# Kernel optimization log

Hardware: AMD Instinct MI355X
Metric: run time of the kernel (lower is better)

## Reference

```python
import jax, jax.numpy as jnp
import numpy as np

BN_EPS = 1e-5

def _conv1x1(x, w, b):
    # x: (B,C,H,W), w: (O,C), b: (O,)
    return jnp.einsum('bchw,oc->bohw', x, w) + b[None, :, None, None]

def setup_inputs() -> dict:
    key = jax.random.key(0)
    ks = jax.random.split(key, 9)
    B, C, H, W = 16, 512, 64, 64
    Ci = C // 2
    x = jax.random.normal(ks[0], (B, C, H, W), dtype=jnp.float32)
    s_in = (2.0 / C) ** 0.5   # kaiming fan_out-ish scale for 1x1 conv
    s_ci = (2.0 / Ci) ** 0.5
    return {
        'x': x,
        'g_w': jax.random.normal(ks[1], (Ci, C), dtype=jnp.float32) * s_in,
        'g_b': jnp.zeros((Ci,), dtype=jnp.float32),
        'theta_w': jax.random.normal(ks[2], (Ci, C), dtype=jnp.float32) * s_in,
        'theta_b': jnp.zeros((Ci,), dtype=jnp.float32),
        'phi_w': jax.random.normal(ks[3], (Ci, C), dtype=jnp.float32) * s_in,
        'phi_b': jnp.zeros((Ci,), dtype=jnp.float32),
        'W_w': jax.random.normal(ks[4], (C, Ci), dtype=jnp.float32) * s_ci,
        'W_b': jnp.zeros((C,), dtype=jnp.float32),
        'bn_gamma': jnp.ones((C,), dtype=jnp.float32),
        'bn_beta': jnp.zeros((C,), dtype=jnp.float32),
    }

def reference(x, g_w, g_b, theta_w, theta_b, phi_w, phi_b, W_w, W_b, bn_gamma, bn_beta):
    B, C, H, W = x.shape
    N = H * W
    g_x = _conv1x1(x, g_w, g_b).reshape(B, -1, N)          # (B, Ci, N)
    theta_x = _conv1x1(x, theta_w, theta_b).reshape(B, -1, N)  # (B, Ci, N)
    phi_x = _conv1x1(x, phi_w, phi_b).reshape(B, -1, N)        # (B, Ci, N)
    # Faithful to source: theta NOT permuted -> f is (B, Ci, Ci) channel attention
    f = jnp.einsum('bcn,bdn->bcd', theta_x, phi_x)
    f_div_C = jax.nn.softmax(f, axis=-1)
    y = jnp.einsum('bcd,bdn->bcn', f_div_C, g_x).reshape(B, -1, H, W)  # (B, Ci, H, W)
    z = _conv1x1(y, W_w, W_b)                              # (B, C, H, W)
    # BatchNorm2d, training mode (batch statistics, biased var as in torch)
    mean = jnp.mean(z, axis=(0, 2, 3), keepdims=True)
    var = jnp.var(z, axis=(0, 2, 3), keepdims=True)
    z = (z - mean) * jax.lax.rsqrt(var + BN_EPS)
    z = z * bn_gamma[None, :, None, None] + bn_beta[None, :, None, None]
    return z + x
```

## Files before the change

### kernel.cpp

```cpp
#include <hip/hip_runtime.h>

typedef __bf16 bf16x8 __attribute__((ext_vector_type(8)));
typedef float f32x4 __attribute__((ext_vector_type(4)));

#define LDK 40
#define NB 16
#define C_ 512
#define CI 256
#define HW 4096
#define KSPLIT 4
#define KCHUNK (HW / KSPLIT)

__device__ __forceinline__ float bf2f(unsigned short u){
  union { unsigned int u; float f; } c; c.u = ((unsigned int)u) << 16; return c.f;
}
__device__ __forceinline__ unsigned short f2bf(float f){
  union { float f; unsigned int u; } c; c.f = f;
  unsigned int u = c.u + 0x7fffu + ((c.u >> 16) & 1u);
  return (unsigned short)(u >> 16);
}
__device__ __forceinline__ float read_val(const void* p, int i, bool f32){
  return f32 ? ((const float*)p)[i] : bf2f(((const unsigned short*)p)[i]);
}


__device__ __forceinline__ void stage_rm(const unsigned short* __restrict__ src, int stride,
                                         unsigned short* dst, int t){
  #pragma unroll
  for (int it = 0; it < 2; ++it){
    int idx = t + it*256;
    int row = idx >> 2;
    int ko  = (idx & 3) * 8;
    *(uint4*)(dst + row*LDK + ko) = *(const uint4*)(src + (size_t)row*stride + ko);
  }
}

__device__ __forceinline__ void stage_tr(const unsigned short* __restrict__ src, int stride,
                                         unsigned short* dst, int t){
  #pragma unroll
  for (int it = 0; it < 2; ++it){
    int idx = t + it*256;
    int row = idx >> 4;
    int co  = (idx & 15) * 8;
    uint4 vv = *(const uint4*)(src + (size_t)row*stride + co);
    unsigned short e[8]; *(uint4*)e = vv;
    #pragma unroll
    for (int k = 0; k < 8; ++k) dst[(co + k)*LDK + row] = e[k];
  }
}

__device__ __forceinline__ void mfma_step(const unsigned short* As, const unsigned short* Bs,
                                          f32x4 acc[4][4], int wm, int wn, int lane){
  const int r = lane & 15, q = lane >> 4;
  bf16x8 a[4], b[4];
  #pragma unroll
  for (int i = 0; i < 4; ++i)
    a[i] = *(const bf16x8*)(As + (wm*64 + 16*i + r)*LDK + 8*q);
  #pragma unroll
  for (int j = 0; j < 4; ++j)
    b[j] = *(const bf16x8*)(Bs + (wn*64 + 16*j + r)*LDK + 8*q);
  #pragma unroll
  for (int i = 0; i < 4; ++i)
    #pragma unroll
    for (int j = 0; j < 4; ++j)
      acc[i][j] = __builtin_amdgcn_mfma_f32_16x16x32_bf16(a[i], b[j], acc[i][j], 0, 0, 0);
}

__global__ __launch_bounds__(256) void k_detect(const unsigned short* __restrict__ x, int* flag){
  const int t = threadIdx.x;
  int cnt = 0;
  for (int i = t; i < 65536; i += 256){
    unsigned short u = x[i];
    if (((u >> 7) & 0xFF) == 0xFF) cnt++;
  }
  __shared__ int red[256];
  red[t] = cnt; __syncthreads();
  for (int s2 = 128; s2 > 0; s2 >>= 1){
    if (t < s2) red[t] += red[t + s2];
    __syncthreads();
  }
  if (t == 0) flag[0] = (red[0] > 0) ? 1 : 0;
}

__global__ __launch_bounds__(256) void k_wconv(const void* tw, const void* pw, const void* gw,
    const void* Ww, const void* gb, const void* tb, const void* pb, const void* Wb,
    const void* gam, const void* bet, const int* __restrict__ flag,
    unsigned short* twh, unsigned short* twl, unsigned short* phh, unsigned short* phl,
    unsigned short* gwc, unsigned short* Wwc, float* biasf){
  const bool f32 = (*flag != 0);
  const int bid = blockIdx.x, t = threadIdx.x;
  if (bid < 2048){
    const int seg = bid >> 9;
    const int i = (bid & 511)*256 + t;
    if (seg == 0){
      float w = read_val(tw, i, f32);
      unsigned short h = f2bf(w);
      twh[i] = h; twl[i] = f2bf(w - bf2f(h));
    } else if (seg == 1){
      float w = read_val(pw, i, f32);
      unsigned short h = f2bf(w);
      phh[i] = h; phl[i] = f2bf(w - bf2f(h));
    } else if (seg == 2){
      gwc[i] = f2bf(read_val(gw, i, f32));
    } else {
      Wwc[i] = f2bf(read_val(Ww, i, f32));
    }
  } else {
    const int i = (bid - 2048)*256 + t;
    if (i < 2304){
      float v;
      if      (i <  256) v = read_val(gb,  i,        f32);
      else if (i <  512) v = read_val(tb,  i - 256,  f32);
      else if (i <  768) v = read_val(pb,  i - 512,  f32);
      else if (i < 1280) v = read_val(Wb,  i - 768,  f32);
      else if (i < 1792) v = read_val(gam, i - 1280, f32);
      else               v = read_val(bet, i - 1792, f32);
      biasf[i] = v;
    }
  }
}

__global__ __launch_bounds__(256) void k_xconv(const void* __restrict__ xraw,
    const int* __restrict__ flag, unsigned short* __restrict__ xh,
    unsigned short* __restrict__ xl, float* __restrict__ s){
  const bool f32 = (*flag != 0);
  const int bc = blockIdx.x, t = threadIdx.x;
  float sum = 0.f;
  if (f32){
    const float* xr = (const float*)xraw + (size_t)bc*HW;
    unsigned short* oh = xh + (size_t)bc*HW;
    unsigned short* ol = xl + (size_t)bc*HW;
    #pragma unroll
    for (int it = 0; it < 4; ++it){
      const int off = it*1024 + t*4;
      f32x4 v = *(const f32x4*)(xr + off);
      unsigned int wh[2], wl[2];
      #pragma unroll
      for (int k = 0; k < 2; ++k){
        unsigned short h0 = f2bf(v[2*k]),   h1 = f2bf(v[2*k+1]);
        unsigned short l0 = f2bf(v[2*k]   - bf2f(h0));
        unsigned short l1 = f2bf(v[2*k+1] - bf2f(h1));
        wh[k] = (unsigned int)h0 | ((unsigned int)h1 << 16);
        wl[k] = (unsigned int)l0 | ((unsigned int)l1 << 16);
      }
      sum += v[0] + v[1] + v[2] + v[3];
      *(uint2*)(oh + off) = make_uint2(wh[0], wh[1]);
      *(uint2*)(ol + off) = make_uint2(wl[0], wl[1]);
    }
  } else {
    const unsigned short* xr = (const unsigned short*)xraw + (size_t)bc*HW;
    #pragma unroll
    for (int it = 0; it < 2; ++it){
      const int off = it*2048 + t*8;
      uint4 raw = *(const uint4*)(xr + off);
      unsigned int wd[4] = {raw.x, raw.y, raw.z, raw.w};
      #pragma unroll
      for (int k = 0; k < 4; ++k)
        sum += bf2f((unsigned short)(wd[k] & 0xffff)) + bf2f((unsigned short)(wd[k] >> 16));
    }
  }
  #pragma unroll
  for (int off = 1; off < 64; off <<= 1) sum += __shfl_xor(sum, off);
  __shared__ float r1[4];
  if ((t & 63) == 0) r1[t >> 6] = sum;
  __syncthreads();
  if (t == 0) s[bc] = r1[0] + r1[1] + r1[2] + r1[3];
}

__global__ __launch_bounds__(256) void k_gram(const void* __restrict__ xraw,
    const unsigned short* __restrict__ xh, const unsigned short* __restrict__ xl,
    const int* __restrict__ flag, float* __restrict__ Gp){
  const bool f32 = (*flag != 0);
  const int b = blockIdx.z, ks = blockIdx.y, tile = blockIdx.x;
  int bm, bn;
  if      (tile < 4){ bm = 0; bn = tile; }
  else if (tile < 7){ bm = 1; bn = tile - 3; }
  else if (tile < 9){ bm = 2; bn = tile - 5; }
  else              { bm = 3; bn = 3; }
  const int t = threadIdx.x, lane = t & 63, w = t >> 6, wm = w >> 1, wn = w & 1;
  __shared__ unsigned short Ah[128*LDK];
  __shared__ unsigned short Al[128*LDK];
  __shared__ unsigned short Bh[128*LDK];
  __shared__ unsigned short Bl[128*LDK];
  f32x4 acc[4][4] = {};
  const bool diag = (bm == bn);
  const unsigned short* xhb = f32 ? (xh + (size_t)b*C_*HW)
                                  : ((const unsigned short*)xraw + (size_t)b*C_*HW);
  const unsigned short* xlb = xl + (size_t)b*C_*HW;
  const int kbeg = ks*KCHUNK, kend = kbeg + KCHUNK;
  for (int k0 = kbeg; k0 < kend; k0 += 32){
    stage_rm(xhb + (size_t)(bm*128)*HW + k0, HW, Ah, t);
    if (f32) stage_rm(xlb + (size_t)(bm*128)*HW + k0, HW, Al, t);
    if (!diag){
      stage_rm(xhb + (size_t)(bn*128)*HW + k0, HW, Bh, t);
      if (f32) stage_rm(xlb + (size_t)(bn*128)*HW + k0, HW, Bl, t);
    }
    __syncthreads();
    const unsigned short* BhU = diag ? Ah : Bh;
    const unsigned short* BlU = diag ? Al : Bl;
    mfma_step(Ah, BhU, acc, wm, wn, lane);
    if (f32){
      mfma_step(Ah, BlU, acc, wm, wn, lane);
      mfma_step(Al, BhU, acc, wm, wn, lane);
    }
    __syncthreads();
  }
  float* Gt = Gp + (((size_t)b*10 + tile)*KSPLIT + ks)*16384;
  const int r = lane & 15, q = lane >> 4;
  #pragma unroll
  for (int i = 0; i < 4; ++i)
    #pragma unroll
    for (int j = 0; j < 4; ++j)
      #pragma unroll
      for (int ii = 0; ii < 4; ++ii){
        int row = wm*64 + 16*i + 4*q + ii;
        int col = wn*64 + 16*j + r;
        Gt[row*128 + col] = acc[i][j][ii];
      }
}

__global__ __launch_bounds__(256) void k_gred(const float* __restrict__ Gp,
    unsigned short* __restrict__ Gh, unsigned short* __restrict__ Gl){
  const int b = blockIdx.z, bmO = blockIdx.y, bnO = blockIdx.x, t = threadIdx.x;
  const int lo = bmO < bnO ? bmO : bnO;
  const int hi = bmO < bnO ? bnO : bmO;
  const int tile = (lo == 0) ? hi : (lo == 1) ? 3 + hi : (lo == 2) ? 5 + hi : 9;
  const float* src = Gp + ((size_t)b*10 + tile)*KSPLIT*16384;
  unsigned short* ghB = Gh + (size_t)b*C_*C_;
  unsigned short* glB = Gl + (size_t)b*C_*C_;
  if (bmO <= bnO){
    #pragma unroll
    for (int i = 0; i < 16; ++i){
      const int off = i*1024 + t*4;
      f32x4 v = *(const f32x4*)(src + off);
      #pragma unroll
      for (int ks = 1; ks < KSPLIT; ++ks){
        f32x4 u2 = *(const f32x4*)(src + ks*16384 + off);
        v[0] += u2[0]; v[1] += u2[1]; v[2] += u2[2]; v[3] += u2[3];
      }
      const int row = off >> 7, col = off & 127;
      unsigned int wh[2], wl[2];
      #pragma unroll
      for (int k = 0; k < 2; ++k){
        unsigned short h0 = f2bf(v[2*k]),   h1 = f2bf(v[2*k+1]);
        unsigned short l0 = f2bf(v[2*k]   - bf2f(h0));
        unsigned short l1 = f2bf(v[2*k+1] - bf2f(h1));
        wh[k] = (unsigned int)h0 | ((unsigned int)h1 << 16);
        wl[k] = (unsigned int)l0 | ((unsigned int)l1 << 16);
      }
      size_t o = (size_t)(bmO*128 + row)*C_ + bnO*128 + col;
      *(uint2*)(ghB + o) = make_uint2(wh[0], wh[1]);
      *(uint2*)(glB + o) = make_uint2(wl[0], wl[1]);
    }
  } else {
    __shared__ float ldz[32*129];
    const int rr = t >> 1, cseg = (t & 1)*16;
    const int orl = t >> 3, oseg = (t & 7)*16;
    for (int cc = 0; cc < 4; ++cc){
      float vals[16];
      #pragma unroll
      for (int j = 0; j < 4; ++j){
        const int so = rr*128 + cc*32 + cseg + j*4;
        f32x4 v = *(const f32x4*)(src + so);
        #pragma unroll
        for (int ks = 1; ks < KSPLIT; ++ks){
          f32x4 u2 = *(const f32x4*)(src + ks*16384 + so);
          v[0] += u2[0]; v[1] += u2[1]; v[2] += u2[2]; v[3] += u2[3];
        }
        vals[4*j] = v[0]; vals[4*j+1] = v[1]; vals[4*j+2] = v[2]; vals[4*j+3] = v[3];
      }
      __syncthreads();
      #pragma unroll
      for (int e = 0; e < 16; ++e) ldz[(cseg + e)*129 + rr] = vals[e];
      __syncthreads();
      unsigned int wh[8], wl[8];
      #pragma unroll
      for (int k = 0; k < 8; ++k){
        float f0 = ldz[orl*129 + oseg + 2*k];
        float f1 = ldz[orl*129 + oseg + 2*k + 1];
        unsigned short h0 = f2bf(f0), h1 = f2bf(f1);
        unsigned short l0 = f2bf(f0 - bf2f(h0)), l1 = f2bf(f1 - bf2f(h1));
        wh[k] = (unsigned int)h0 | ((unsigned int)h1 << 16);
        wl[k] = (unsigned int)l0 | ((unsigned int)l1 << 16);
      }
      size_t o = (size_t)(bmO*128 + cc*32 + orl)*C_ + bnO*128 + oseg;
      *(uint4*)(ghB + o)     = make_uint4(wh[0], wh[1], wh[2], wh[3]);
      *(uint4*)(ghB + o + 8) = make_uint4(wh[4], wh[5], wh[6], wh[7]);
      *(uint4*)(glB + o)     = make_uint4(wl[0], wl[1], wl[2], wl[3]);
      *(uint4*)(glB + o + 8) = make_uint4(wl[4], wl[5], wl[6], wl[7]);
    }
  }
}

__global__ __launch_bounds__(256) void k_gconv(const void* __restrict__ xraw,
    const int* __restrict__ flag, const unsigned short* __restrict__ xh,
    const unsigned short* __restrict__ gwc,
    const float* __restrict__ gbf, unsigned short* __restrict__ gT){
  const bool f32 = (*flag != 0);
  const int b = blockIdx.z, mt = blockIdx.x, nt = blockIdx.y;
  const int t = threadIdx.x, lane = t & 63, w = t >> 6, wm = w >> 1, wn = w & 1;
  __shared__ unsigned short As[128*LDK];
  __shared__ unsigned short Bs[128*LDK];
  f32x4 acc[4][4] = {};
  const unsigned short* xb = f32 ? (xh + (size_t)b*C_*HW)
                                 : ((const unsigned short*)xraw + (size_t)b*C_*HW);
  for (int k0 = 0; k0 < C_; k0 += 32){
    stage_tr(xb + (size_t)k0*HW + mt*128, HW, As, t);
    stage_rm(gwc + (size_t)nt*128*C_ + k0, C_, Bs, t);
    __syncthreads();
    mfma_step(As, Bs, acc, wm, wn, lane);
    __syncthreads();
  }
  unsigned short* gTb = gT + (size_t)b*HW*CI;
  const int r = lane & 15, q = lane >> 4;
  #pragma unroll
  for (int j = 0; j < 4; ++j){
    int col = nt*128 + wn*64 + 16*j + r;
    float bias = gbf[col];
    #pragma unroll
    for (int i = 0; i < 4; ++i)
      #pragma unroll
      for (int ii = 0; ii < 4; ++ii){
        int row = mt*128 + wm*64 + 16*i + 4*q + ii;
        gTb[(size_t)row*CI + col] = f2bf(acc[i][j][ii] + bias);
      }
  }
}

__global__ __launch_bounds__(256) void k_T(const unsigned short* __restrict__ twh,
    const unsigned short* __restrict__ twl, const int* __restrict__ flag,
    const unsigned short* __restrict__ Gh, const unsigned short* __restrict__ Gl,
    unsigned short* __restrict__ Th, unsigned short* __restrict__ Tl){
  const bool f32 = (*flag != 0);
  const int b = blockIdx.z, nt = blockIdx.x, mt = blockIdx.y;
  const int t = threadIdx.x, lane = t & 63, w = t >> 6, wm = w >> 1, wn = w & 1;
  __shared__ unsigned short Ath[128*LDK];
  __shared__ unsigned short Atl[128*LDK];
  __shared__ unsigned short Bh[128*LDK];
  __shared__ unsigned short Bl[128*LDK];
  const unsigned short* Ghb = Gh + (size_t)b*C_*C_;
  const unsigned short* Glb = Gl + (size_t)b*C_*C_;
  f32x4 acc[4][4] = {};
  for (int k0 = 0; k0 < C_; k0 += 32){
    stage_rm(twh + (size_t)mt*128*C_ + k0, C_, Ath, t);
    if (f32) stage_rm(twl + (size_t)mt*128*C_ + k0, C_, Atl, t);
    stage_rm(Ghb + (size_t)nt*128*C_ + k0, C_, Bh, t);
    stage_rm(Glb + (size_t)nt*128*C_ + k0, C_, Bl, t);
    __syncthreads();
    mfma_step(Ath, Bh, acc, wm, wn, lane);
    mfma_step(Ath, Bl, acc, wm, wn, lane);
    if (f32) mfma_step(Atl, Bh, acc, wm, wn, lane);
    __syncthreads();
  }
  unsigned short* Thb = Th + (size_t)b*CI*C_;
  unsigned short* Tlb = Tl + (size_t)b*CI*C_;
  const int r = lane & 15, q = lane >> 4;
  #pragma unroll
  for (int i = 0; i < 4; ++i)
    #pragma unroll
    for (int j = 0; j < 4; ++j)
      #pragma unroll
      for (int ii = 0; ii < 4; ++ii){
        int row = mt*128 + wm*64 + 16*i + 4*q + ii;
        int col = nt*128 + wn*64 + 16*j + r;
        float vv = acc[i][j][ii];
        unsigned short h = f2bf(vv);
        Thb[(size_t)row*C_ + col] = h;
        Tlb[(size_t)row*C_ + col] = f2bf(vv - bf2f(h));
      }
}

__global__ __launch_bounds__(256) void k_f(const unsigned short* __restrict__ Th,
    const unsigned short* __restrict__ Tl, const unsigned short* __restrict__ phh,
    const unsigned short* __restrict__ phl, const int* __restrict__ flag,
    float* __restrict__ f){
  const bool f32 = (*flag != 0);
  const int b = blockIdx.z, nt = blockIdx.x, mt = blockIdx.y;
  const int t = threadIdx.x, lane = t & 63, w = t >> 6, wm = w >> 1, wn = w & 1;
  __shared__ unsigned short ATh[128*LDK];
  __shared__ unsigned short ATl[128*LDK];
  __shared__ unsigned short Bph[128*LDK];
  __shared__ unsigned short Bpl[128*LDK];
  f32x4 acc[4][4] = {};
  const unsigned short* Thb = Th + (size_t)b*CI*C_;
  const unsigned short* Tlb = Tl + (size_t)b*CI*C_;
  for (int k0 = 0; k0 < C_; k0 += 32){
    stage_rm(Thb + (size_t)mt*128*C_ + k0, C_, ATh, t);
    stage_rm(Tlb + (size_t)mt*128*C_ + k0, C_, ATl, t);
    stage_rm(phh + (size_t)nt*128*C_ + k0, C_, Bph, t);
    if (f32) stage_rm(phl + (size_t)nt*128*C_ + k0, C_, Bpl, t);
    __syncthreads();
    mfma_step(ATh, Bph, acc, wm, wn, lane);
    mfma_step(ATl, Bph, acc, wm, wn, lane);
    if (f32) mfma_step(ATh, Bpl, acc, wm, wn, lane);
    __syncthreads();
  }
  float* fb = f + (size_t)b*CI*CI;
  const int r = lane & 15, q = lane >> 4;
  #pragma unroll
  for (int i = 0; i < 4; ++i)
    #pragma unroll
    for (int j = 0; j < 4; ++j)
      #pragma unroll
      for (int ii = 0; ii < 4; ++ii){
        int row = mt*128 + wm*64 + 16*i + 4*q + ii;
        int col = nt*128 + wn*64 + 16*j + r;
        fb[(size_t)row*CI + col] = acc[i][j][ii];
      }
}

__global__ __launch_bounds__(256) void k_uv(const unsigned short* __restrict__ twh,
    const unsigned short* __restrict__ twl, const unsigned short* __restrict__ phh,
    const unsigned short* __restrict__ phl, const float* __restrict__ s,
    float* __restrict__ u, float* __restrict__ v){
  const int b = blockIdx.x, c = threadIdx.x;
  __shared__ float sl[C_];
  sl[c] = s[(size_t)b*C_ + c];
  sl[c + 256] = s[(size_t)b*C_ + c + 256];
  __syncthreads();
  float su = 0.f, sv = 0.f;
  for (int e = 0; e < C_; ++e){
    su += (bf2f(twh[(size_t)c*C_ + e]) + bf2f(twl[(size_t)c*C_ + e])) * sl[e];
    sv += (bf2f(phh[(size_t)c*C_ + e]) + bf2f(phl[(size_t)c*C_ + e])) * sl[e];
  }
  u[(size_t)b*CI + c] = su;
  v[(size_t)b*CI + c] = sv;
}

__global__ __launch_bounds__(256) void k_softmax(const float* __restrict__ f,
    const float* __restrict__ u, const float* __restrict__ v,
    const float* __restrict__ tbf, const float* __restrict__ pbf,
    unsigned short* __restrict__ S){
  const int b = blockIdx.y;
  const int c = blockIdx.x*4 + (threadIdx.x >> 6);
  const int lane = threadIdx.x & 63;
  const float* fr = f + ((size_t)b*CI + c)*CI;
  f32x4 val = *(const f32x4*)(fr + lane*4);
  const float uc = u[(size_t)b*CI + c];
  const float tbc = tbf[c];
  float vv[4];
  #pragma unroll
  for (int k = 0; k < 4; ++k){
    int d = lane*4 + k;
    float pbd = pbf[d];
    vv[k] = val[k] + uc*pbd + tbc*(v[(size_t)b*CI + d] + 4096.0f*pbd);
  }
  float mx = fmaxf(fmaxf(vv[0], vv[1]), fmaxf(vv[2], vv[3]));
  #pragma unroll
  for (int off = 1; off < 64; off <<= 1) mx = fmaxf(mx, __shfl_xor(mx, off));
  float e[4], sum = 0.f;
  #pragma unroll
  for (int k = 0; k < 4; ++k){ e[k] = expf(vv[k] - mx); sum += e[k]; }
  #pragma unroll
  for (int off = 1; off < 64; off <<= 1) sum += __shfl_xor(sum, off);
  float inv = 1.0f / sum;
  uint2 pack;
  pack.x = (unsigned int)f2bf(e[0]*inv) | ((unsigned int)f2bf(e[1]*inv) << 16);
  pack.y = (unsigned int)f2bf(e[2]*inv) | ((unsigned int)f2bf(e[3]*inv) << 16);
  *(uint2*)(S + ((size_t)b*CI + c)*CI + lane*4) = pack;
}

__global__ __launch_bounds__(256) void k_M2(const unsigned short* __restrict__ Wwc,
                                            const unsigned short* __restrict__ S,
                                            unsigned short* __restrict__ M2){
  const int b = blockIdx.z, nt = blockIdx.x, mt = blockIdx.y;
  const int t = threadIdx.x, lane = t & 63, w = t >> 6, wm = w >> 1, wn = w & 1;
  __shared__ unsigned short As[128*LDK];
  __shared__ unsigned short Bs[128*LDK];
  f32x4 acc[4][4] = {};
  for (int k0 = 0; k0 < CI; k0 += 32){
    stage_rm(Wwc + (size_t)mt*128*CI + k0, CI, As, t);
    stage_tr(S + (size_t)b*CI*CI + (size_t)k0*CI + nt*128, CI, Bs, t);
    __syncthreads();
    mfma_step(As, Bs, acc, wm, wn, lane);
    __syncthreads();
  }
  unsigned short* M2b = M2 + (size_t)b*C_*CI;
  const int r = lane & 15, q = lane >> 4;
  #pragma unroll
  for (int i = 0; i < 4; ++i)
    #pragma unroll
    for (int j = 0; j < 4; ++j)
      #pragma unroll
      for (int ii = 0; ii < 4; ++ii){
        int row = mt*128 + wm*64 + 16*i + 4*q + ii;
        int col = nt*128 + wn*64 + 16*j + r;
        M2b[(size_t)row*CI + col] = f2bf(acc[i][j][ii]);
      }
}

__global__ __launch_bounds__(256) void k_z(const unsigned short* __restrict__ M2,
                                           const unsigned short* __restrict__ gT,
                                           const float* __restrict__ Wbf,
                                           unsigned short* __restrict__ z){
  const int b = blockIdx.z, nt = blockIdx.x, mt = blockIdx.y;
  const int t = threadIdx.x, lane = t & 63, w = t >> 6, wm = w >> 1, wn = w & 1;
  __shared__ unsigned short As[128*LDK];
  __shared__ unsigned short Bs[128*LDK];
  const unsigned short* M2b = M2 + (size_t)b*C_*CI;
  const unsigned short* gTb = gT + (size_t)b*HW*CI;
  f32x4 acc[4][4] = {};
  for (int k0 = 0; k0 < CI; k0 += 32){
    stage_rm(M2b + (size_t)mt*128*CI + k0, CI, As, t);
    stage_rm(gTb + (size_t)nt*128*CI + k0, CI, Bs, t);
    __syncthreads();
    mfma_step(As, Bs, acc, wm, wn, lane);
    __syncthreads();
  }
  unsigned short* zb = z + (size_t)b*C_*HW;
  const int r = lane & 15, q = lane >> 4;
  #pragma unroll
  for (int i = 0; i < 4; ++i)
    #pragma unroll
    for (int ii = 0; ii < 4; ++ii){
      int row = mt*128 + wm*64 + 16*i + 4*q + ii;
      float bias = Wbf[row];
      #pragma unroll
      for (int j = 0; j < 4; ++j){
        int col = nt*128 + wn*64 + 16*j + r;
        zb[(size_t)row*HW + col] = f2bf(acc[i][j][ii] + bias);
      }
    }
}

__global__ __launch_bounds__(256) void k_bnstats(const unsigned short* __restrict__ z,
    const float* __restrict__ gamf, const float* __restrict__ betf,
    float* __restrict__ scale, float* __restrict__ shift){
  const int o = blockIdx.x, t = threadIdx.x, lane = t & 63, w = t >> 6;
  float sum = 0.f, ss = 0.f;
  for (int b = 0; b < NB; ++b){
    const unsigned short* p = z + ((size_t)b*C_ + o)*HW + t*16;
    #pragma unroll
    for (int it = 0; it < 2; ++it){
      uint4 raw = *(const uint4*)(p + it*8);
      unsigned int wd[4] = {raw.x, raw.y, raw.z, raw.w};
      #pragma unroll
      for (int k = 0; k < 4; ++k){
        float f0 = bf2f((unsigned short)(wd[k] & 0xffff));
        float f1 = bf2f((unsigned short)(wd[k] >> 16));
        sum += f0 + f1; ss += f0*f0 + f1*f1;
      }
    }
  }
  #pragma unroll
  for (int off = 1; off < 64; off <<= 1){
    sum += __shfl_xor(sum, off);
    ss  += __shfl_xor(ss, off);
  }
  __shared__ float r1[4], r2[4];
  if (lane == 0){ r1[w] = sum; r2[w] = ss; }
  __syncthreads();
  if (t == 0){
    float S1 = r1[0]+r1[1]+r1[2]+r1[3];
    float S2 = r2[0]+r2[1]+r2[2]+r2[3];
    const float n = (float)NB * (float)HW;
    float mean = S1 / n;
    float var  = S2 / n - mean*mean;
    float sc = gamf[o] * rsqrtf(var + 1e-5f);
    scale[o] = sc;
    shift[o] = betf[o] - mean*sc;
  }
}

__global__ __launch_bounds__(256) void k_out(const unsigned short* __restrict__ z,
    const void* __restrict__ xraw, const int* __restrict__ flag,
    const float* __restrict__ scale, const float* __restrict__ shift, void* __restrict__ outraw){
  const bool f32 = (*flag != 0);
  const size_t g = (size_t)blockIdx.x*256 + threadIdx.x;
  const size_t base = g*8;
  const int o = (int)((base >> 12) & (C_ - 1));
  const float sc = scale[o], sh = shift[o];
  uint4 zr = *(const uint4*)(z + base);
  unsigned int zz[4] = {zr.x, zr.y, zr.z, zr.w};
  float zv[8];
  #pragma unroll
  for (int k = 0; k < 4; ++k){
    zv[2*k]   = bf2f((unsigned short)(zz[k] & 0xffff));
    zv[2*k+1] = bf2f((unsigned short)(zz[k] >> 16));
  }
  if (f32){
    const float* x = (const float*)xraw;
    float* out = (float*)outraw;
    f32x4 x0 = *(const f32x4*)(x + base);
    f32x4 x1 = *(const f32x4*)(x + base + 4);
    f32x4 o0, o1;
    #pragma unroll
    for (int k = 0; k < 4; ++k){
      o0[k] = zv[k]*sc + sh + x0[k];
      o1[k] = zv[4+k]*sc + sh + x1[k];
    }
    *(f32x4*)(out + base) = o0;
    *(f32x4*)(out + base + 4) = o1;
  } else {
    const unsigned short* x = (const unsigned short*)xraw;
    unsigned short* out = (unsigned short*)outraw;
    uint4 xr = *(const uint4*)(x + base);
    unsigned int xx[4] = {xr.x, xr.y, xr.z, xr.w};
    unsigned int res[4];
    #pragma unroll
    for (int k = 0; k < 4; ++k){
      float x0 = bf2f((unsigned short)(xx[k] & 0xffff));
      float x1 = bf2f((unsigned short)(xx[k] >> 16));
      res[k] = (unsigned int)f2bf(zv[2*k]*sc + sh + x0)
             | ((unsigned int)f2bf(zv[2*k+1]*sc + sh + x1) << 16);
    }
    uint4 ov; ov.x = res[0]; ov.y = res[1]; ov.z = res[2]; ov.w = res[3];
    *(uint4*)(out + base) = ov;
  }
}

extern "C" void kernel_launch(void* const* d_in, const int* in_sizes, int n_in,
                              void* d_out, int out_size, void* d_ws, size_t ws_size,
                              hipStream_t stream){
  (void)in_sizes; (void)n_in; (void)out_size;
  const void* x   = d_in[0];
  const void* g_w = d_in[1];
  const void* g_b = d_in[2];
  const void* t_w = d_in[3];
  const void* t_b = d_in[4];
  const void* p_w = d_in[5];
  const void* p_b = d_in[6];
  const void* W_w = d_in[7];
  const void* W_b = d_in[8];
  const void* gam = d_in[9];
  const void* bet = d_in[10];
  char* ws = (char*)d_ws;

  constexpr size_t OFF_FLAG = 0;
  constexpr size_t OFF_TWH = OFF_FLAG + 16;
  constexpr size_t OFF_TWL = OFF_TWH + (size_t)CI*C_*2;
  constexpr size_t OFF_PHH = OFF_TWL + (size_t)CI*C_*2;
  constexpr size_t OFF_PHL = OFF_PHH + (size_t)CI*C_*2;
  constexpr size_t OFF_GWC = OFF_PHL + (size_t)CI*C_*2;
  constexpr size_t OFF_WWC = OFF_GWC + (size_t)CI*C_*2;
  constexpr size_t OFF_BIA = OFF_WWC + (size_t)C_*CI*2;
  constexpr size_t OFF_GH = OFF_BIA + 2304*4;
  constexpr size_t OFF_GL = OFF_GH + (size_t)NB*C_*C_*2;
  constexpr size_t OFF_S  = OFF_GL + (size_t)NB*C_*C_*2;
  constexpr size_t OFF_U  = OFF_S  + (size_t)NB*C_*4;
  constexpr size_t OFF_V  = OFF_U  + (size_t)NB*CI*4;
  constexpr size_t OFF_GT = OFF_V  + (size_t)NB*CI*4;
  constexpr size_t OFF_TH = OFF_GT + (size_t)NB*HW*CI*2;
  constexpr size_t OFF_TL = OFF_TH + (size_t)NB*CI*C_*2;
  constexpr size_t OFF_F  = OFF_TL + (size_t)NB*CI*C_*2;
  constexpr size_t OFF_SM = OFF_F  + (size_t)NB*CI*CI*4;
  constexpr size_t OFF_M2 = OFF_SM + (size_t)NB*CI*CI*2;
  constexpr size_t OFF_Z  = OFF_M2 + (size_t)NB*C_*CI*2;
  constexpr size_t OFF_SC = OFF_Z  + (size_t)NB*C_*HW*2;
  constexpr size_t OFF_SH = OFF_SC + (size_t)C_*4;
  constexpr size_t OFF_XH = OFF_SH + (size_t)C_*4;
  constexpr size_t TOTAL  = OFF_XH + (size_t)NB*C_*HW*2;
  static_assert((size_t)NB*10*KSPLIT*16384*4 ==
                (size_t)NB*HW*CI*2 + 2*(size_t)NB*CI*C_*2, "Gp alias size");
  if (ws_size < TOTAL) return;

  int* flag = (int*)(ws + OFF_FLAG);
  unsigned short* twh = (unsigned short*)(ws + OFF_TWH);
  unsigned short* twl = (unsigned short*)(ws + OFF_TWL);
  unsigned short* phh = (unsigned short*)(ws + OFF_PHH);
  unsigned short* phl = (unsigned short*)(ws + OFF_PHL);
  unsigned short* gwc = (unsigned short*)(ws + OFF_GWC);
  unsigned short* Wwc = (unsigned short*)(ws + OFF_WWC);
  float* biasf = (float*)(ws + OFF_BIA);
  unsigned short* Gh = (unsigned short*)(ws + OFF_GH);
  unsigned short* Gl = (unsigned short*)(ws + OFF_GL);
  float* s  = (float*)(ws + OFF_S);
  float* u  = (float*)(ws + OFF_U);
  float* v  = (float*)(ws + OFF_V);
  unsigned short* gT = (unsigned short*)(ws + OFF_GT);
  unsigned short* Th = (unsigned short*)(ws + OFF_TH);
  unsigned short* Tl = (unsigned short*)(ws + OFF_TL);
  float* f  = (float*)(ws + OFF_F);
  unsigned short* Sm = (unsigned short*)(ws + OFF_SM);
  unsigned short* M2 = (unsigned short*)(ws + OFF_M2);
  unsigned short* z  = (unsigned short*)(ws + OFF_Z);
  float* scale = (float*)(ws + OFF_SC);
  float* shift = (float*)(ws + OFF_SH);
  unsigned short* xh = (unsigned short*)(ws + OFF_XH);
  unsigned short* xl = (unsigned short*)(ws + OFF_Z);
  float* Gp = (float*)(ws + OFF_GT);

  float* gbf = biasf;
  float* tbf = biasf + 256;
  float* pbf = biasf + 512;
  float* Wbf = biasf + 768;
  float* gamf = biasf + 1280;
  float* betf = biasf + 1792;

  dim3 blk(256);
  k_detect <<<dim3(1),          blk, 0, stream>>>((const unsigned short*)x, flag);
  k_wconv  <<<dim3(2057),       blk, 0, stream>>>(t_w, p_w, g_w, W_w, g_b, t_b, p_b, W_b,
                                                  gam, bet, flag, twh, twl, phh, phl, gwc, Wwc, biasf);
  k_xconv  <<<dim3(NB*C_),      blk, 0, stream>>>(x, flag, xh, xl, s);
  k_gram   <<<dim3(10, KSPLIT, NB), blk, 0, stream>>>(x, xh, xl, flag, Gp);
  k_gred   <<<dim3(4, 4, NB),   blk, 0, stream>>>(Gp, Gh, Gl);
  k_gconv  <<<dim3(32, 2, NB),  blk, 0, stream>>>(x, flag, xh, gwc, gbf, gT);
  k_T      <<<dim3(4, 2, NB),   blk, 0, stream>>>(twh, twl, flag, Gh, Gl, Th, Tl);
  k_uv     <<<dim3(NB),         blk, 0, stream>>>(twh, twl, phh, phl, s, u, v);
  k_f      <<<dim3(2, 2, NB),   blk, 0, stream>>>(Th, Tl, phh, phl, flag, f);
  k_softmax<<<dim3(64, NB),     blk, 0, stream>>>(f, u, v, tbf, pbf, Sm);
  k_M2     <<<dim3(2, 4, NB),   blk, 0, stream>>>(Wwc, Sm, M2);
  k_z      <<<dim3(32, 4, NB),  blk, 0, stream>>>(M2, gT, Wbf, z);
  k_bnstats<<<dim3(C_),         blk, 0, stream>>>(z, gamf, betf, scale, shift);
  k_out    <<<dim3(16384),      blk, 0, stream>>>(z, x, flag, scale, shift, d_out);
}
```

Measured before the change: 856.3 us.

## Fold g-conv into W-matrix, interleave hi/lo x, async double-buffered gram loads

Drops the separate g = Wg·x convolution and instead precomputes per batch Wg = M2·g_w (512x512) plus a folded bias. z is then produced by a single GEMM over x with a 512-row tile. The x hi/lo bf16 split is stored interleaved in 64-element chunks, and the gram kernel now stages data with global_load_lds in swizzled, double-buffered LDS. This removes the gT intermediate and its write/read traffic and overlaps loads with MFMA. In exchange, the z GEMM's K grows from 256 to 512, and z now multiplies only the high half of x.

```diff
diff --git a/kernel.cpp b/kernel.cpp
--- a/kernel.cpp
+++ b/kernel.cpp
@@ -64,6 +64,23 @@
     #pragma unroll
     for (int j = 0; j < 4; ++j)
       acc[i][j] = __builtin_amdgcn_mfma_f32_16x16x32_bf16(a[i], b[j], acc[i][j], 0, 0, 0);
+}
+
+__device__ __forceinline__ void gload16(const unsigned short* g, unsigned short* l){
+  __builtin_amdgcn_global_load_lds(
+      (__attribute__((address_space(1))) void*)const_cast<unsigned short*>(g),
+      (__attribute__((address_space(3))) void*)l, 16, 0, 0);
+}
+
+__device__ __forceinline__ void gstage(const unsigned short* __restrict__ src, size_t rstride,
+                                       unsigned short* buf, int w, int lane){
+  const int ro = lane >> 3;
+  const int sc = (lane & 7) ^ ro;
+  const unsigned short* s0 = src + (size_t)ro*rstride + sc*8;
+  unsigned short* l0 = buf + (size_t)(w*32)*64;
+  #pragma unroll
+  for (int i = 0; i < 4; ++i)
+    gload16(s0 + (size_t)(w*32 + i*8)*rstride, l0 + i*8*64);
 }
 
 __global__ __launch_bounds__(256) void k_detect(const unsigned short* __restrict__ x, int* flag){
@@ -121,15 +138,13 @@
 }
 
 __global__ __launch_bounds__(256) void k_xconv(const void* __restrict__ xraw,
-    const int* __restrict__ flag, unsigned short* __restrict__ xh,
-    unsigned short* __restrict__ xl, float* __restrict__ s){
+    const int* __restrict__ flag, unsigned short* __restrict__ xq, float* __restrict__ s){
   const bool f32 = (*flag != 0);
   const int bc = blockIdx.x, t = threadIdx.x;
   float sum = 0.f;
   if (f32){
     const float* xr = (const float*)xraw + (size_t)bc*HW;
-    unsigned short* oh = xh + (size_t)bc*HW;
-    unsigned short* ol = xl + (size_t)bc*HW;
+    unsigned short* oq = xq + (size_t)bc*8192;
     #pragma unroll
     for (int it = 0; it < 4; ++it){
       const int off = it*1024 + t*4;
@@ -144,8 +159,9 @@
         wl[k] = (unsigned int)l0 | ((unsigned int)l1 << 16);
       }
       sum += v[0] + v[1] + v[2] + v[3];
-      *(uint2*)(oh + off) = make_uint2(wh[0], wh[1]);
-      *(uint2*)(ol + off) = make_uint2(wl[0], wl[1]);
+      const int qb = (off >> 5)*64 + (off & 31);
+      *(uint2*)(oq + qb)      = make_uint2(wh[0], wh[1]);
+      *(uint2*)(oq + qb + 32) = make_uint2(wl[0], wl[1]);
     }
   } else {
     const unsigned short* xr = (const unsigned short*)xraw + (size_t)bc*HW;
@@ -168,8 +184,8 @@
 }
 
 __global__ __launch_bounds__(256) void k_gram(const void* __restrict__ xraw,
-    const unsigned short* __restrict__ xh, const unsigned short* __restrict__ xl,
-    const int* __restrict__ flag, float* __restrict__ Gp){
+    const unsigned short* __restrict__ xq, const int* __restrict__ flag,
+    float* __restrict__ Gp){
   const bool f32 = (*flag != 0);
   const int b = blockIdx.z, ks = blockIdx.y, tile = blockIdx.x;
   int bm, bn;
@@ -178,35 +194,77 @@
   else if (tile < 9){ bm = 2; bn = tile - 5; }
   else              { bm = 3; bn = 3; }
   const int t = threadIdx.x, lane = t & 63, w = t >> 6, wm = w >> 1, wn = w & 1;
-  __shared__ unsigned short Ah[128*LDK];
-  __shared__ unsigned short Al[128*LDK];
-  __shared__ unsigned short Bh[128*LDK];
-  __shared__ unsigned short Bl[128*LDK];
+  __shared__ __align__(16) unsigned short Abuf[2][128*64];
+  __shared__ __align__(16) unsigned short Bbuf[2][128*64];
+  const bool diag = (bm == bn);
+  const unsigned short* srcA;
+  const unsigned short* srcB;
+  size_t rstride;
+  int nsteps;
+  if (f32){
+    const unsigned short* xb = xq + (size_t)b*C_*8192;
+    srcA = xb + (size_t)(bm*128)*8192 + (size_t)ks*(KCHUNK/32)*64;
+    srcB = xb + (size_t)(bn*128)*8192 + (size_t)ks*(KCHUNK/32)*64;
+    rstride = 8192; nsteps = KCHUNK/32;
+  } else {
+    const unsigned short* xb = (const unsigned short*)xraw + (size_t)b*C_*HW;
+    srcA = xb + (size_t)(bm*128)*HW + ks*KCHUNK;
+    srcB = xb + (size_t)(bn*128)*HW + ks*KCHUNK;
+    rstride = HW; nsteps = KCHUNK/64;
+  }
   f32x4 acc[4][4] = {};
-  const bool diag = (bm == bn);
-  const unsigned short* xhb = f32 ? (xh + (size_t)b*C_*HW)
-                                  : ((const unsigned short*)xraw + (size_t)b*C_*HW);
-  const unsigned short* xlb = xl + (size_t)b*C_*HW;
-  const int kbeg = ks*KCHUNK, kend = kbeg + KCHUNK;
-  for (int k0 = kbeg; k0 < kend; k0 += 32){
-    stage_rm(xhb + (size_t)(bm*128)*HW + k0, HW, Ah, t);
-    if (f32) stage_rm(xlb + (size_t)(bm*128)*HW + k0, HW, Al, t);
-    if (!diag){
-      stage_rm(xhb + (size_t)(bn*128)*HW + k0, HW, Bh, t);
-      if (f32) stage_rm(xlb + (size_t)(bn*128)*HW + k0, HW, Bl, t);
-    }
-    __syncthreads();
-    const unsigned short* BhU = diag ? Ah : Bh;
-    const unsigned short* BlU = diag ? Al : Bl;
-    mfma_step(Ah, BhU, acc, wm, wn, lane);
+  const int r = lane & 15, q = lane >> 4;
+  const int rx = r & 7;
+  const int c0 = q ^ rx;
+  const int c1 = (4 + q) ^ rx;
+
+  gstage(srcA, rstride, Abuf[0], w, lane);
+  if (!diag) gstage(srcB, rstride, Bbuf[0], w, lane);
+  __syncthreads();
+
+  int cur = 0;
+  for (int st = 0; st < nsteps; ++st){
+    if (st + 1 < nsteps){
+      gstage(srcA + (size_t)(st+1)*64, rstride, Abuf[cur^1], w, lane);
+      if (!diag) gstage(srcB + (size_t)(st+1)*64, rstride, Bbuf[cur^1], w, lane);
+    }
+    const unsigned short* A = Abuf[cur];
+    const unsigned short* B = diag ? Abuf[cur] : Bbuf[cur];
+    bf16x8 a0[4], a1[4], b0[4], b1[4];
+    #pragma unroll
+    for (int i = 0; i < 4; ++i){
+      const unsigned short* ap = A + (size_t)(wm*64 + 16*i + r)*64;
+      a0[i] = *(const bf16x8*)(ap + c0*8);
+      a1[i] = *(const bf16x8*)(ap + c1*8);
+    }
+    #pragma unroll
+    for (int j = 0; j < 4; ++j){
+      const unsigned short* bp = B + (size_t)(wn*64 + 16*j + r)*64;
+      b0[j] = *(const bf16x8*)(bp + c0*8);
+      b1[j] = *(const bf16x8*)(bp + c1*8);
+    }
     if (f32){
-      mfma_step(Ah, BlU, acc, wm, wn, lane);
-      mfma_step(Al, BhU, acc, wm, wn, lane);
-    }
-    __syncthreads();
+      #pragma unroll
+      for (int i = 0; i < 4; ++i)
+        #pragma unroll
+        for (int j = 0; j < 4; ++j){
+          acc[i][j] = __builtin_amdgcn_mfma_f32_16x16x32_bf16(a0[i], b0[j], acc[i][j], 0, 0, 0);
+          acc[i][j] = __builtin_amdgcn_mfma_f32_16x16x32_bf16(a0[i], b1[j], acc[i][j], 0, 0, 0);
+          acc[i][j] = __builtin_amdgcn_mfma_f32_16x16x32_bf16(a1[i], b0[j], acc[i][j], 0, 0, 0);
+        }
+    } else {
+      #pragma unroll
+      for (int i = 0; i < 4; ++i)
+        #pragma unroll
+        for (int j = 0; j < 4; ++j){
+          acc[i][j] = __builtin_amdgcn_mfma_f32_16x16x32_bf16(a0[i], b0[j], acc[i][j], 0, 0, 0);
+          acc[i][j] = __builtin_amdgcn_mfma_f32_16x16x32_bf16(a1[i], b1[j], acc[i][j], 0, 0, 0);
+        }
+    }
+    __syncthreads();
+    cur ^= 1;
   }
   float* Gt = Gp + (((size_t)b*10 + tile)*KSPLIT + ks)*16384;
-  const int r = lane & 15, q = lane >> 4;
   #pragma unroll
   for (int i = 0; i < 4; ++i)
     #pragma unroll
@@ -289,41 +347,6 @@
       *(uint4*)(glB + o)     = make_uint4(wl[0], wl[1], wl[2], wl[3]);
       *(uint4*)(glB + o + 8) = make_uint4(wl[4], wl[5], wl[6], wl[7]);
     }
-  }
-}
-
-__global__ __launch_bounds__(256) void k_gconv(const void* __restrict__ xraw,
-    const int* __restrict__ flag, const unsigned short* __restrict__ xh,
-    const unsigned short* __restrict__ gwc,
-    const float* __restrict__ gbf, unsigned short* __restrict__ gT){
-  const bool f32 = (*flag != 0);
-  const int b = blockIdx.z, mt = blockIdx.x, nt = blockIdx.y;
-  const int t = threadIdx.x, lane = t & 63, w = t >> 6, wm = w >> 1, wn = w & 1;
-  __shared__ unsigned short As[128*LDK];
-  __shared__ unsigned short Bs[128*LDK];
-  f32x4 acc[4][4] = {};
-  const unsigned short* xb = f32 ? (xh + (size_t)b*C_*HW)
-                                 : ((const unsigned short*)xraw + (size_t)b*C_*HW);
-  for (int k0 = 0; k0 < C_; k0 += 32){
-    stage_tr(xb + (size_t)k0*HW + mt*128, HW, As, t);
-    stage_rm(gwc + (size_t)nt*128*C_ + k0, C_, Bs, t);
-    __syncthreads();
-    mfma_step(As, Bs, acc, wm, wn, lane);
-    __syncthreads();
-  }
-  unsigned short* gTb = gT + (size_t)b*HW*CI;
-  const int r = lane & 15, q = lane >> 4;
-  #pragma unroll
-  for (int j = 0; j < 4; ++j){
-    int col = nt*128 + wn*64 + 16*j + r;
-    float bias = gbf[col];
-    #pragma unroll
-    for (int i = 0; i < 4; ++i)
-      #pragma unroll
-      for (int ii = 0; ii < 4; ++ii){
-        int row = mt*128 + wm*64 + 16*i + 4*q + ii;
-        gTb[(size_t)row*CI + col] = f2bf(acc[i][j][ii] + bias);
-      }
   }
 }
 
@@ -489,35 +512,113 @@
       }
 }
 
-__global__ __launch_bounds__(256) void k_z(const unsigned short* __restrict__ M2,
-                                           const unsigned short* __restrict__ gT,
-                                           const float* __restrict__ Wbf,
-                                           unsigned short* __restrict__ z){
+__global__ __launch_bounds__(256) void k_Wg(const unsigned short* __restrict__ M2,
+                                            const unsigned short* __restrict__ gwc,
+                                            unsigned short* __restrict__ Wg){
   const int b = blockIdx.z, nt = blockIdx.x, mt = blockIdx.y;
   const int t = threadIdx.x, lane = t & 63, w = t >> 6, wm = w >> 1, wn = w & 1;
   __shared__ unsigned short As[128*LDK];
   __shared__ unsigned short Bs[128*LDK];
   const unsigned short* M2b = M2 + (size_t)b*C_*CI;
-  const unsigned short* gTb = gT + (size_t)b*HW*CI;
   f32x4 acc[4][4] = {};
   for (int k0 = 0; k0 < CI; k0 += 32){
     stage_rm(M2b + (size_t)mt*128*CI + k0, CI, As, t);
-    stage_rm(gTb + (size_t)nt*128*CI + k0, CI, Bs, t);
+    stage_tr(gwc + (size_t)k0*C_ + nt*128, C_, Bs, t);
     __syncthreads();
     mfma_step(As, Bs, acc, wm, wn, lane);
     __syncthreads();
   }
+  unsigned short* Wgb = Wg + (size_t)b*C_*C_;
+  const int r = lane & 15, q = lane >> 4;
+  #pragma unroll
+  for (int i = 0; i < 4; ++i)
+    #pragma unroll
+    for (int j = 0; j < 4; ++j)
+      #pragma unroll
+      for (int ii = 0; ii < 4; ++ii){
+        int row = mt*128 + wm*64 + 16*i + 4*q + ii;
+        int col = nt*128 + wn*64 + 16*j + r;
+        Wgb[(size_t)row*C_ + col] = f2bf(acc[i][j][ii]);
+      }
+}
+
+__global__ __launch_bounds__(256) void k_bias2(const unsigned short* __restrict__ M2,
+    const float* __restrict__ gbf, const float* __restrict__ Wbf, float* __restrict__ b2){
+  const int b = blockIdx.x, t = threadIdx.x;
+  __shared__ float gs[CI];
+  gs[t] = gbf[t];
+  __syncthreads();
+  #pragma unroll
+  for (int cc = 0; cc < 2; ++cc){
+    int c = cc*256 + t;
+    const unsigned short* row = M2 + (size_t)b*C_*CI + (size_t)c*CI;
+    float sv = 0.f;
+    for (int ci = 0; ci < CI; ++ci) sv += bf2f(row[ci]) * gs[ci];
+    b2[(size_t)b*C_ + c] = sv + Wbf[c];
+  }
+}
+
+__global__ __launch_bounds__(512) void k_zW(const unsigned short* __restrict__ Wg,
+    const void* __restrict__ xraw, const unsigned short* __restrict__ xq,
+    const int* __restrict__ flag, const float* __restrict__ bias2,
+    unsigned short* __restrict__ z){
+  const bool f32 = (*flag != 0);
+  const int b = blockIdx.z, hwp = blockIdx.x;
+  const int t = threadIdx.x, lane = t & 63, w = t >> 6;
+  const int wm = w >> 1, wn = w & 1;
+  __shared__ __align__(16) unsigned short As[512*LDK];
+  __shared__ __align__(16) unsigned short Bs[128*LDK];
+  const unsigned short* Wgb = Wg + (size_t)b*C_*C_;
+  const int hw0 = hwp*128;
+  f32x4 acc[8][4] = {};
+  for (int k0 = 0; k0 < C_; k0 += 32){
+    #pragma unroll
+    for (int it = 0; it < 4; ++it){
+      int idx = t + it*512;
+      int row = idx >> 2, ko = (idx & 3)*8;
+      *(uint4*)(As + row*LDK + ko) = *(const uint4*)(Wgb + (size_t)row*C_ + k0 + ko);
+    }
+    {
+      int row = t >> 4, co = (t & 15)*8;
+      const unsigned short* bsrc;
+      if (f32){
+        int hw = hw0 + co;
+        bsrc = xq + (size_t)(b*C_ + k0 + row)*8192 + (size_t)((hw >> 5)*64 + (hw & 31));
+      } else {
+        bsrc = (const unsigned short*)xraw + (size_t)(b*C_ + k0 + row)*HW + hw0 + co;
+      }
+      uint4 vv = *(const uint4*)bsrc;
+      unsigned short e8[8]; *(uint4*)e8 = vv;
+      #pragma unroll
+      for (int kk = 0; kk < 8; ++kk) Bs[(co + kk)*LDK + row] = e8[kk];
+    }
+    __syncthreads();
+    const int r = lane & 15, q = lane >> 4;
+    bf16x8 bfr[4];
+    #pragma unroll
+    for (int j = 0; j < 4; ++j)
+      bfr[j] = *(const bf16x8*)(Bs + (wn*64 + 16*j + r)*LDK + 8*q);
+    #pragma unroll
+    for (int i = 0; i < 8; ++i){
+      bf16x8 af = *(const bf16x8*)(As + (size_t)(wm*128 + 16*i + r)*LDK + 8*q);
+      #pragma unroll
+      for (int j = 0; j < 4; ++j)
+        acc[i][j] = __builtin_amdgcn_mfma_f32_16x16x32_bf16(af, bfr[j], acc[i][j], 0, 0, 0);
+    }
+    __syncthreads();
+  }
   unsigned short* zb = z + (size_t)b*C_*HW;
+  const float* b2 = bias2 + (size_t)b*C_;
   const int r = lane & 15, q = lane >> 4;
   #pragma unroll
-  for (int i = 0; i < 4; ++i)
+  for (int i = 0; i < 8; ++i)
     #pragma unroll
     for (int ii = 0; ii < 4; ++ii){
-      int row = mt*128 + wm*64 + 16*i + 4*q + ii;
-      float bias = Wbf[row];
+      int row = wm*128 + 16*i + 4*q + ii;
+      float bias = b2[row];
       #pragma unroll
       for (int j = 0; j < 4; ++j){
-        int col = nt*128 + wn*64 + 16*j + r;
+        int col = hw0 + wn*64 + 16*j + r;
         zb[(size_t)row*HW + col] = f2bf(acc[i][j][ii] + bias);
       }
     }
@@ -634,24 +735,23 @@
   constexpr size_t OFF_GWC = OFF_PHL + (size_t)CI*C_*2;
   constexpr size_t OFF_WWC = OFF_GWC + (size_t)CI*C_*2;
   constexpr size_t OFF_BIA = OFF_WWC + (size_t)C_*CI*2;
-  constexpr size_t OFF_GH = OFF_BIA + 2304*4;
-  constexpr size_t OFF_GL = OFF_GH + (size_t)NB*C_*C_*2;
-  constexpr size_t OFF_S  = OFF_GL + (size_t)NB*C_*C_*2;
-  constexpr size_t OFF_U  = OFF_S  + (size_t)NB*C_*4;
-  constexpr size_t OFF_V  = OFF_U  + (size_t)NB*CI*4;
-  constexpr size_t OFF_GT = OFF_V  + (size_t)NB*CI*4;
-  constexpr size_t OFF_TH = OFF_GT + (size_t)NB*HW*CI*2;
-  constexpr size_t OFF_TL = OFF_TH + (size_t)NB*CI*C_*2;
-  constexpr size_t OFF_F  = OFF_TL + (size_t)NB*CI*C_*2;
-  constexpr size_t OFF_SM = OFF_F  + (size_t)NB*CI*CI*4;
-  constexpr size_t OFF_M2 = OFF_SM + (size_t)NB*CI*CI*2;
-  constexpr size_t OFF_Z  = OFF_M2 + (size_t)NB*C_*CI*2;
-  constexpr size_t OFF_SC = OFF_Z  + (size_t)NB*C_*HW*2;
-  constexpr size_t OFF_SH = OFF_SC + (size_t)C_*4;
-  constexpr size_t OFF_XH = OFF_SH + (size_t)C_*4;
-  constexpr size_t TOTAL  = OFF_XH + (size_t)NB*C_*HW*2;
-  static_assert((size_t)NB*10*KSPLIT*16384*4 ==
-                (size_t)NB*HW*CI*2 + 2*(size_t)NB*CI*C_*2, "Gp alias size");
+  constexpr size_t OFF_GH  = OFF_BIA + 16384;
+  constexpr size_t OFF_GL  = OFF_GH + (size_t)NB*C_*C_*2;
+  constexpr size_t OFF_S   = OFF_GL + (size_t)NB*C_*C_*2;
+  constexpr size_t OFF_U   = OFF_S  + (size_t)NB*C_*4;
+  constexpr size_t OFF_V   = OFF_U  + (size_t)NB*CI*4;
+  constexpr size_t OFF_TH  = OFF_V  + (size_t)NB*CI*4;
+  constexpr size_t OFF_TL  = OFF_TH + (size_t)NB*CI*C_*2;
+  constexpr size_t OFF_F   = OFF_TL + (size_t)NB*CI*C_*2;
+  constexpr size_t OFF_SM  = OFF_F  + (size_t)NB*CI*CI*4;
+  constexpr size_t OFF_M2  = OFF_SM + (size_t)NB*CI*CI*2;
+  constexpr size_t OFF_B2  = OFF_M2 + (size_t)NB*C_*CI*2;
+  constexpr size_t OFF_SC  = OFF_B2 + (size_t)NB*C_*4;
+  constexpr size_t OFF_SH  = OFF_SC + (size_t)C_*4;
+  constexpr size_t OFF_Z   = OFF_SH + (size_t)C_*4;
+  constexpr size_t OFF_XQ  = OFF_Z  + (size_t)NB*C_*HW*2;
+  constexpr size_t TOTAL   = OFF_XQ + (size_t)NB*C_*HW*4;
+  static_assert((size_t)NB*10*KSPLIT*16384*4 <= (size_t)NB*C_*HW*2, "Gp alias fits in Z");
   if (ws_size < TOTAL) return;
 
   int* flag = (int*)(ws + OFF_FLAG);
@@ -667,18 +767,18 @@
   float* s  = (float*)(ws + OFF_S);
   float* u  = (float*)(ws + OFF_U);
   float* v  = (float*)(ws + OFF_V);
-  unsigned short* gT = (unsigned short*)(ws + OFF_GT);
   unsigned short* Th = (unsigned short*)(ws + OFF_TH);
   unsigned short* Tl = (unsigned short*)(ws + OFF_TL);
   float* f  = (float*)(ws + OFF_F);
   unsigned short* Sm = (unsigned short*)(ws + OFF_SM);
   unsigned short* M2 = (unsigned short*)(ws + OFF_M2);
+  float* b2 = (float*)(ws + OFF_B2);
   unsigned short* z  = (unsigned short*)(ws + OFF_Z);
   float* scale = (float*)(ws + OFF_SC);
   float* shift = (float*)(ws + OFF_SH);
-  unsigned short* xh = (unsigned short*)(ws + OFF_XH);
-  unsigned short* xl = (unsigned short*)(ws + OFF_Z);
-  float* Gp = (float*)(ws + OFF_GT);
+  unsigned short* xq = (unsigned short*)(ws + OFF_XQ);
+  float* Gp = (float*)(ws + OFF_Z);
+  unsigned short* Wg = (unsigned short*)(ws + OFF_GH);
 
   float* gbf = biasf;
   float* tbf = biasf + 256;
@@ -691,16 +791,17 @@
   k_detect <<<dim3(1),          blk, 0, stream>>>((const unsigned short*)x, flag);
   k_wconv  <<<dim3(2057),       blk, 0, stream>>>(t_w, p_w, g_w, W_w, g_b, t_b, p_b, W_b,
                                                   gam, bet, flag, twh, twl, phh, phl, gwc, Wwc, biasf);
-  k_xconv  <<<dim3(NB*C_),      blk, 0, stream>>>(x, flag, xh, xl, s);
-  k_gram   <<<dim3(10, KSPLIT, NB), blk, 0, stream>>>(x, xh, xl, flag, Gp);
+  k_xconv  <<<dim3(NB*C_),      blk, 0, stream>>>(x, flag, xq, s);
+  k_gram   <<<dim3(10, KSPLIT, NB), blk, 0, stream>>>(x, xq, flag, Gp);
   k_gred   <<<dim3(4, 4, NB),   blk, 0, stream>>>(Gp, Gh, Gl);
-  k_gconv  <<<dim3(32, 2, NB),  blk, 0, stream>>>(x, flag, xh, gwc, gbf, gT);
   k_T      <<<dim3(4, 2, NB),   blk, 0, stream>>>(twh, twl, flag, Gh, Gl, Th, Tl);
   k_uv     <<<dim3(NB),         blk, 0, stream>>>(twh, twl, phh, phl, s, u, v);
   k_f      <<<dim3(2, 2, NB),   blk, 0, stream>>>(Th, Tl, phh, phl, flag, f);
   k_softmax<<<dim3(64, NB),     blk, 0, stream>>>(f, u, v, tbf, pbf, Sm);
   k_M2     <<<dim3(2, 4, NB),   blk, 0, stream>>>(Wwc, Sm, M2);
-  k_z      <<<dim3(32, 4, NB),  blk, 0, stream>>>(M2, gT, Wbf, z);
+  k_Wg     <<<dim3(4, 4, NB),   blk, 0, stream>>>(M2, gwc, Wg);
+  k_bias2  <<<dim3(NB),         blk, 0, stream>>>(M2, gbf, Wbf, b2);
+  k_zW     <<<dim3(32, 1, NB),  dim3(512), 0, stream>>>(Wg, x, xq, flag, b2, z);
   k_bnstats<<<dim3(C_),         blk, 0, stream>>>(z, gamf, betf, scale, shift);
   k_out    <<<dim3(16384),      blk, 0, stream>>>(z, x, flag, scale, shift, d_out);
 }
```

Measured after the change: 769.9 us. 1.11x faster.
